# Optimization experiments

Hardware: AMD Instinct MI355X
Metric: run time of the kernel (lower is better)

## Reference

```python
import jax, jax.numpy as jnp
import numpy as np

S, NL = 64, 5000          # num_sequences, num_labels
PD, LD = 1024, 768        # protein / label embedding dims
DIM, OD = 512, 512        # latent_dim, output_dim


def setup_inputs() -> dict:
    key = jax.random.key(0)
    ks = jax.random.split(key, 8)
    sc = lambda f: 1.0 / np.sqrt(f).astype(np.float32)
    return {
        "P_f": jax.random.normal(ks[0], (S, PD), jnp.float32),
        "label_emb": jax.random.normal(ks[1], (NL, LD), jnp.float32),
        "W_p": jax.random.normal(ks[2], (DIM, PD), jnp.float32) * sc(PD),
        "W_l": jax.random.normal(ks[3], (DIM, LD), jnp.float32) * sc(LD),
        "W1": jax.random.normal(ks[4], (OD, 2 * DIM), jnp.float32) * sc(2 * DIM),
        "b1": jnp.zeros((OD,), jnp.float32),
        "W2": jax.random.normal(ks[5], (OD, OD), jnp.float32) * sc(OD),
        "b2": jnp.zeros((OD,), jnp.float32),
        "W3": jax.random.normal(ks[6], (1, OD), jnp.float32) * sc(OD),
        "b3": jnp.zeros((1,), jnp.float32),
        "L": jnp.arange(NL, dtype=jnp.int64),
    }


def reference(P_f, label_emb, W_p, W_l, W1, b1, W2, b2, W3, b3, L):
    # label lookup (cached_label_embeddings(L)) + linear projections
    L_f = label_emb[L]                      # [NL, LD]
    P_e = P_f @ W_p.T                       # [S, DIM]
    L_e = L_f @ W_l.T                       # [NL, DIM]
    # joint cat([P_e_expanded, L_e_expanded]) @ W1.T  ==  P-side + L-side GEMMs,
    # broadcast-summed (avoids materializing the [S*NL, 2*DIM] concat)
    hp = P_e @ W1[:, :DIM].T                # [S, OD]
    hl = L_e @ W1[:, DIM:].T                # [NL, OD]
    h = jax.nn.relu(hp[:, None, :] + hl[None, :, :] + b1)   # [S, NL, OD]
    h = jax.nn.relu(jnp.einsum("snd,od->sno", h, W2) + b2)  # [S, NL, OD]
    logits = jnp.einsum("sno,o->sn", h, W3[0]) + b3[0]      # [S, NL]
    return logits
```

## Files before the change

### kernel.cpp

```cpp
#include <hip/hip_runtime.h>
#include <hip/hip_bf16.h>

typedef short short8 __attribute__((ext_vector_type(8)));
typedef float f32x4 __attribute__((ext_vector_type(4)));

#define S_   64
#define NL_  5000
#define PD_  1024
#define LD_  768
#define DIM_ 512
#define OD_  512

#define BK     32
#define KSTEPS 16
#define NT_M   79
#define HL_RT  157

__device__ __forceinline__ ushort f2bf(float f) {
    union { float f; unsigned u; } v; v.f = f;
    unsigned r = v.u + 0x7fffu + ((v.u >> 16) & 1u);
    return (ushort)(r >> 16);
}
__device__ __forceinline__ float bf2f(ushort h) {
    union { unsigned u; float f; } v; v.u = ((unsigned)h) << 16;
    return v.f;
}
__device__ __forceinline__ int swz(int row, int kslot) {
    return (row * 64 + kslot * 16) ^ (((row >> 1) & 7) << 4);
}
__device__ __forceinline__ void glds16(const void* g, void* l) {
    __builtin_amdgcn_global_load_lds(
        (const __attribute__((address_space(1))) void*)g,
        (__attribute__((address_space(3))) void*)l, 16, 0, 0);
}

__device__ __forceinline__ void proj8(
    float* Af , const float* __restrict__ A, int lda, int K,
    const float* __restrict__ W, int ldw, const float* __restrict__ bias,
    float* __restrict__ C, int o0, int t) {
    const int s = t & 63, og = t >> 6;
    const int oA = o0 + og * 2, oB = oA + 1;
    float acc0 = 0.f, acc1 = 0.f;
    for (int ck = 0; ck < K; ck += 256) {
        __syncthreads();
#pragma unroll
        for (int it = 0; it < 16; it++) {
            int r = it * 4 + (t >> 6);
            float4 v = *(const float4*)(A + (size_t)r * lda + ck + (t & 63) * 4);
            *(float4*)(Af + r * 258 + (t & 63) * 4) = v;
        }
        __syncthreads();
        const float* w0 = W + (size_t)oA * ldw + ck;
        const float* w1 = W + (size_t)oB * ldw + ck;
        const float* ar = Af + s * 258;
#pragma unroll 8
        for (int k4 = 0; k4 < 64; k4++) {
            f32x4 a4 = *(const f32x4*)(ar + k4 * 4);
            float4 v0 = *(const float4*)(w0 + k4 * 4);
            float4 v1 = *(const float4*)(w1 + k4 * 4);
            acc0 += a4[0] * v0.x + a4[1] * v0.y + a4[2] * v0.z + a4[3] * v0.w;
            acc1 += a4[0] * v1.x + a4[1] * v1.y + a4[2] * v1.z + a4[3] * v1.w;
        }
    }
    C[s * DIM_ + oA] = acc0 + (bias ? bias[oA] : 0.f);
    C[s * DIM_ + oB] = acc1 + (bias ? bias[oB] : 0.f);
}

__global__ __launch_bounds__(256) void k_pre1(
    const float* __restrict__ W2, const float* __restrict__ W_l,
    const float* __restrict__ W1, const float* __restrict__ P_f,
    const float* __restrict__ W_p,
    char* __restrict__ panel, ushort* __restrict__ MlT, float* __restrict__ P_e) {
    __shared__ float lbuf[64 * 258];
    int b = blockIdx.x, t = threadIdx.x;
    if (b < 128) {
        int c = b * 256 + t;
        int o = c >> 6, rem = c & 63, kt = rem >> 2, kslot = rem & 3;
        const float* src = W2 + o * DIM_ + kt * BK + kslot * 8;
        float4 v0 = *(const float4*)src;
        float4 v1 = *(const float4*)(src + 4);
        union { ushort u[8]; short8 v; } pk;
        pk.u[0] = f2bf(v0.x); pk.u[1] = f2bf(v0.y); pk.u[2] = f2bf(v0.z); pk.u[3] = f2bf(v0.w);
        pk.u[4] = f2bf(v1.x); pk.u[5] = f2bf(v1.y); pk.u[6] = f2bf(v1.z); pk.u[7] = f2bf(v1.w);
        *(short8*)(panel + kt * 32768 + swz(o, kslot)) = pk.v;
    } else if (b < 320) {
        float (*w1r)[DIM_] = (float (*)[DIM_])lbuf;
        int bx = b - 128;
        int o0 = (bx / 3) * 8;
        int ld = (bx % 3) * 256 + t;
        for (int i = t; i < 8 * DIM_; i += 256)
            w1r[i >> 9][i & 511] = W1[(o0 + (i >> 9)) * (2 * DIM_) + DIM_ + (i & 511)];
        __syncthreads();
        float acc[8] = {};
        for (int dim = 0; dim < DIM_; dim++) {
            float wl = W_l[dim * LD_ + ld];
#pragma unroll
            for (int oi = 0; oi < 8; oi++) acc[oi] += w1r[oi][dim] * wl;
        }
#pragma unroll
        for (int oi = 0; oi < 8; oi++) MlT[(o0 + oi) * LD_ + ld] = f2bf(acc[oi]);
    } else {
        proj8(lbuf, P_f, PD_, PD_, W_p, PD_, nullptr, P_e, (b - 320) * 8, t);
    }
}

__global__ __launch_bounds__(256) void k_pre2(
    const float* __restrict__ P_e, const float* __restrict__ W1,
    const float* __restrict__ b1, const float* __restrict__ emb,
    const int* __restrict__ L, const ushort* __restrict__ MlT,
    float* __restrict__ hpb, ushort* __restrict__ hlB) {
    __shared__ float lbuf[64 * 258];
    int b = blockIdx.x, t = threadIdx.x;
    if (b < 64) {
        proj8(lbuf, P_e, DIM_, DIM_, W1, 2 * DIM_, b1, hpb, b * 8, t);
    } else {
        int hb = b - 64;
        int rblk = hb % HL_RT, oh = hb / HL_RT;
        int r0 = rblk * 32;
        int w = t >> 6, l = t & 63, lg = l >> 4, ll = l & 15;
        const float* arow[2];
#pragma unroll
        for (int mt = 0; mt < 2; mt++) {
            int r = r0 + mt * 16 + ll;
            if (r >= NL_) r = NL_ - 1;
            arow[mt] = emb + (size_t)L[r] * LD_ + lg * 8;
        }
        f32x4 acc[2][4] = {};
        for (int k = 0; k < LD_; k += 32) {
            short8 a[2], bf[4];
#pragma unroll
            for (int mt = 0; mt < 2; mt++) {
                float4 v0 = *(const float4*)(arow[mt] + k);
                float4 v1 = *(const float4*)(arow[mt] + k + 4);
                union { ushort u[8]; short8 v; } pk;
                pk.u[0] = f2bf(v0.x); pk.u[1] = f2bf(v0.y);
                pk.u[2] = f2bf(v0.z); pk.u[3] = f2bf(v0.w);
                pk.u[4] = f2bf(v1.x); pk.u[5] = f2bf(v1.y);
                pk.u[6] = f2bf(v1.z); pk.u[7] = f2bf(v1.w);
                a[mt] = pk.v;
            }
#pragma unroll
            for (int ot = 0; ot < 4; ot++) {
                int o = oh * 256 + w * 64 + ot * 16 + ll;
                bf[ot] = *(const short8*)(MlT + o * LD_ + k + lg * 8);
            }
#pragma unroll
            for (int mt = 0; mt < 2; mt++)
#pragma unroll
                for (int ot = 0; ot < 4; ot++)
                    acc[mt][ot] = __builtin_amdgcn_mfma_f32_16x16x32_bf16(a[mt], bf[ot], acc[mt][ot], 0, 0, 0);
        }
#pragma unroll
        for (int mt = 0; mt < 2; mt++)
#pragma unroll
            for (int ot = 0; ot < 4; ot++)
#pragma unroll
                for (int reg = 0; reg < 4; reg++) {
                    int r = r0 + mt * 16 + lg * 4 + reg;
                    if (r < NL_)
                        hlB[(size_t)r * DIM_ + oh * 256 + w * 64 + ot * 16 + ll] = f2bf(acc[mt][ot][reg]);
                }
    }
}

__global__ __launch_bounds__(512, 2) void k_main2(
    const ushort* __restrict__ hlB, const float* __restrict__ hpb,
    const char* __restrict__ panel, const float* __restrict__ b2,
    const float* __restrict__ W3, const float* __restrict__ b3,
    float* __restrict__ out) {
    __shared__ f32x4 ldsv[7168];
    char* lds = (char*)ldsv;
    const int t = threadIdx.x;
    const int n0 = blockIdx.x * 64, s0 = blockIdx.y * 2;
    const int w = t >> 6, lane = t & 63, lg = lane >> 4, ll = lane & 15;
    const int wr = w >> 2, wc = w & 3;

    const int arow = t >> 2, akslot = t & 3;
    int an = n0 + (arow & 63); if (an >= NL_) an = NL_ - 1;
    const ushort* hlsrc = hlB + (size_t)an * DIM_ + akslot * 8;
    const float*  hpsrc = hpb + (s0 + (arow >> 6)) * DIM_ + akslot * 8;
    const int awz = swz(arow, akslot);

    int aoffS[4], boffS[8];
#pragma unroll
    for (int mt = 0; mt < 4; mt++) aoffS[mt] = swz(wr * 64 + mt * 16 + ll, lg);
#pragma unroll
    for (int ot = 0; ot < 8; ot++) boffS[ot] = swz(wc * 128 + ot * 16 + ll, lg);

    f32x4 acc[4][8] = {};

    auto stageB = [&](int kt, int buf) {
        const char* base = panel + kt * 32768 + w * 4096 + (lane << 4);
        char* ldsB = lds + 16384 + buf * 32768 + w * 4096;
#pragma unroll
        for (int r = 0; r < 4; r++) glds16(base + r * 1024, ldsB + r * 1024);
    };
    auto packA = [&](int buf, short8 hv, float4 p0, float4 p1) {
        float hp8[8] = { p0.x, p0.y, p0.z, p0.w, p1.x, p1.y, p1.z, p1.w };
        float x[8];
#pragma unroll
        for (int e = 0; e < 8; e++) {
            float s = bf2f((ushort)hv[e]) + hp8[e];
            x[e] = s > 0.f ? s : 0.f;
        }
        union { __hip_bfloat162 h2[4]; short8 v; } pk;
#pragma unroll
        for (int e = 0; e < 4; e++)
            pk.h2[e] = __float22bfloat162_rn(make_float2(x[2 * e], x[2 * e + 1]));
        *(short8*)(lds + buf * 8192 + awz) = pk.v;
    };

    {
        short8 hv = *(const short8*)(hlsrc);
        float4 p0 = *(const float4*)(hpsrc);
        float4 p1 = *(const float4*)(hpsrc + 4);
        __builtin_amdgcn_sched_barrier(0);
        stageB(0, 0);
        stageB(1, 1);
        __builtin_amdgcn_sched_barrier(0);
        packA(0, hv, p0, p1);
        asm volatile("s_waitcnt vmcnt(4) lgkmcnt(0)" ::: "memory");
        __builtin_amdgcn_s_barrier();
    }

    for (int kt = 0; kt < KSTEPS; kt++) {
        short8 hv; float4 p0, p1;
        if (kt + 1 < KSTEPS) {
            hv = *(const short8*)(hlsrc + (kt + 1) * BK);
            p0 = *(const float4*)(hpsrc + (kt + 1) * BK);
            p1 = *(const float4*)(hpsrc + (kt + 1) * BK + 4);
        }
        __builtin_amdgcn_sched_barrier(0);
        if (kt + 2 < KSTEPS) stageB(kt + 2, (kt + 2) % 3);
        __builtin_amdgcn_sched_barrier(0);
        const char* A = lds + (kt & 1) * 8192;
        const char* B = lds + 16384 + (kt % 3) * 32768;
        short8 a[4], b[8];
#pragma unroll
        for (int mt = 0; mt < 4; mt++) a[mt] = *(const short8*)(A + aoffS[mt]);
#pragma unroll
        for (int ot = 0; ot < 8; ot++) b[ot] = *(const short8*)(B + boffS[ot]);
        __builtin_amdgcn_s_setprio(1);
#pragma unroll
        for (int mt = 0; mt < 4; mt++)
#pragma unroll
            for (int ot = 0; ot < 8; ot++)
                acc[mt][ot] = __builtin_amdgcn_mfma_f32_16x16x32_bf16(a[mt], b[ot], acc[mt][ot], 0, 0, 0);
        __builtin_amdgcn_s_setprio(0);
        if (kt + 1 < KSTEPS) packA((kt + 1) & 1, hv, p0, p1);
        asm volatile("s_waitcnt vmcnt(4) lgkmcnt(0)" ::: "memory");
        __builtin_amdgcn_s_barrier();
    }

    float* logit = (float*)lds;
    if (t < 128) logit[t] = 0.f;
    __syncthreads();
#pragma unroll
    for (int mt = 0; mt < 4; mt++) {
        float p4[4] = { 0.f, 0.f, 0.f, 0.f };
#pragma unroll
        for (int ot = 0; ot < 8; ot++) {
            int o = wc * 128 + ot * 16 + ll;
            float bb = b2[o], w3 = W3[o];
#pragma unroll
            for (int reg = 0; reg < 4; reg++) {
                float v = acc[mt][ot][reg] + bb;
                v = v > 0.f ? v : 0.f;
                p4[reg] += v * w3;
            }
        }
#pragma unroll
        for (int m = 1; m < 16; m <<= 1)
#pragma unroll
            for (int reg = 0; reg < 4; reg++) p4[reg] += __shfl_xor(p4[reg], m, 64);
        if (ll == 0)
#pragma unroll
            for (int reg = 0; reg < 4; reg++)
                atomicAdd(&logit[wr * 64 + mt * 16 + lg * 4 + reg], p4[reg]);
    }
    __syncthreads();
    if (t < 128) {
        int n = n0 + (t & 63);
        int s = s0 + (t >> 6);
        if (n < NL_) out[(size_t)s * NL_ + n] = logit[t] + b3[0];
    }
}

extern "C" void kernel_launch(void* const* d_in, const int* in_sizes, int n_in,
                              void* d_out, int out_size, void* d_ws, size_t ws_size,
                              hipStream_t stream) {
    const float* P_f = (const float*)d_in[0];
    const float* emb = (const float*)d_in[1];
    const float* W_p = (const float*)d_in[2];
    const float* W_l = (const float*)d_in[3];
    const float* W1  = (const float*)d_in[4];
    const float* b1  = (const float*)d_in[5];
    const float* W2  = (const float*)d_in[6];
    const float* b2  = (const float*)d_in[7];
    const float* W3  = (const float*)d_in[8];
    const float* b3  = (const float*)d_in[9];
    const int*   L   = (const int*)d_in[10];
    float* out = (float*)d_out;

    char* ws = (char*)d_ws;
    size_t off = 0;
    auto alloc = [&](size_t bytes) {
        void* p = ws + off;
        off = (off + bytes + 255) & ~(size_t)255;
        return p;
    };
    char*   panel = (char*)alloc((size_t)KSTEPS * 32768);
    ushort* MlT   = (ushort*)alloc((size_t)OD_ * LD_ * 2);
    float*  P_e   = (float*)alloc((size_t)S_ * DIM_ * 4);
    float*  hpb   = (float*)alloc((size_t)S_ * DIM_ * 4);
    ushort* hlB   = (ushort*)alloc((size_t)NL_ * DIM_ * 2);

    k_pre1<<<384, 256, 0, stream>>>(W2, W_l, W1, P_f, W_p, panel, MlT, P_e);
    k_pre2<<<378, 256, 0, stream>>>(P_e, W1, b1, emb, L, MlT, hpb, hlB);
    k_main2<<<dim3(NT_M, 32), 512, 0, stream>>>(hlB, hpb, panel, b2, W3, b3, out);
}
```

Baseline: 275.7 us.

## Load W2 panel fragments directly from global into registers, dropping LDS staging

The W2 bf16 panel is re-laid out so that each MFMA B-fragment is a contiguous 16-byte-per-lane chunk. The main kernel then reads B fragments straight from global memory (likely L2-resident) into registers, split into two register-buffered halves and prefetched one k-step ahead, instead of staging them through a triple-buffered LDS ring with global_load_lds. This cuts LDS use from 112KB to 16KB per block, which may allow more resident blocks, and removes the LDS B traffic. The cost is global-load latency sitting on the MFMA critical path, plus redundant per-wave global reads of the same panel.

```diff
diff --git a/kernel.cpp b/kernel.cpp
--- a/kernel.cpp
+++ b/kernel.cpp
@@ -27,11 +27,6 @@
 }
 __device__ __forceinline__ int swz(int row, int kslot) {
     return (row * 64 + kslot * 16) ^ (((row >> 1) & 7) << 4);
-}
-__device__ __forceinline__ void glds16(const void* g, void* l) {
-    __builtin_amdgcn_global_load_lds(
-        (const __attribute__((address_space(1))) void*)g,
-        (__attribute__((address_space(3))) void*)l, 16, 0, 0);
 }
 
 __device__ __forceinline__ void proj8(
@@ -82,7 +77,7 @@
         union { ushort u[8]; short8 v; } pk;
         pk.u[0] = f2bf(v0.x); pk.u[1] = f2bf(v0.y); pk.u[2] = f2bf(v0.z); pk.u[3] = f2bf(v0.w);
         pk.u[4] = f2bf(v1.x); pk.u[5] = f2bf(v1.y); pk.u[6] = f2bf(v1.z); pk.u[7] = f2bf(v1.w);
-        *(short8*)(panel + kt * 32768 + swz(o, kslot)) = pk.v;
+        *(short8*)(panel + kt * 32768 + (o >> 4) * 1024 + kslot * 256 + (o & 15) * 16) = pk.v;
     } else if (b < 320) {
         float (*w1r)[DIM_] = (float (*)[DIM_])lbuf;
         int bx = b - 128;
@@ -168,7 +163,7 @@
     const char* __restrict__ panel, const float* __restrict__ b2,
     const float* __restrict__ W3, const float* __restrict__ b3,
     float* __restrict__ out) {
-    __shared__ f32x4 ldsv[7168];
+    __shared__ f32x4 ldsv[1024];
     char* lds = (char*)ldsv;
     const int t = threadIdx.x;
     const int n0 = blockIdx.x * 64, s0 = blockIdx.y * 2;
@@ -181,20 +176,11 @@
     const float*  hpsrc = hpb + (s0 + (arow >> 6)) * DIM_ + akslot * 8;
     const int awz = swz(arow, akslot);
 
-    int aoffS[4], boffS[8];
-#pragma unroll
-    for (int mt = 0; mt < 4; mt++) aoffS[mt] = swz(wr * 64 + mt * 16 + ll, lg);
-#pragma unroll
-    for (int ot = 0; ot < 8; ot++) boffS[ot] = swz(wc * 128 + ot * 16 + ll, lg);
+    const int abase = swz(wr * 64 + ll, lg);
+    const char* bbase = panel + (wc * 8) * 1024 + lane * 16;
 
     f32x4 acc[4][8] = {};
 
-    auto stageB = [&](int kt, int buf) {
-        const char* base = panel + kt * 32768 + w * 4096 + (lane << 4);
-        char* ldsB = lds + 16384 + buf * 32768 + w * 4096;
-#pragma unroll
-        for (int r = 0; r < 4; r++) glds16(base + r * 1024, ldsB + r * 1024);
-    };
     auto packA = [&](int buf, short8 hv, float4 p0, float4 p1) {
         float hp8[8] = { p0.x, p0.y, p0.z, p0.w, p1.x, p1.y, p1.z, p1.w };
         float x[8];
@@ -214,41 +200,47 @@
         short8 hv = *(const short8*)(hlsrc);
         float4 p0 = *(const float4*)(hpsrc);
         float4 p1 = *(const float4*)(hpsrc + 4);
-        __builtin_amdgcn_sched_barrier(0);
-        stageB(0, 0);
-        stageB(1, 1);
-        __builtin_amdgcn_sched_barrier(0);
         packA(0, hv, p0, p1);
-        asm volatile("s_waitcnt vmcnt(4) lgkmcnt(0)" ::: "memory");
+        asm volatile("s_waitcnt lgkmcnt(0)" ::: "memory");
         __builtin_amdgcn_s_barrier();
     }
+    short8 bq0[4], bq1[4];
+#pragma unroll
+    for (int j = 0; j < 4; j++) bq0[j] = *(const short8*)(bbase + j * 1024);
 
     for (int kt = 0; kt < KSTEPS; kt++) {
+        const char* bkt = bbase + kt * 32768;
         short8 hv; float4 p0, p1;
         if (kt + 1 < KSTEPS) {
             hv = *(const short8*)(hlsrc + (kt + 1) * BK);
             p0 = *(const float4*)(hpsrc + (kt + 1) * BK);
             p1 = *(const float4*)(hpsrc + (kt + 1) * BK + 4);
         }
-        __builtin_amdgcn_sched_barrier(0);
-        if (kt + 2 < KSTEPS) stageB(kt + 2, (kt + 2) % 3);
-        __builtin_amdgcn_sched_barrier(0);
         const char* A = lds + (kt & 1) * 8192;
-        const char* B = lds + 16384 + (kt % 3) * 32768;
-        short8 a[4], b[8];
-#pragma unroll
-        for (int mt = 0; mt < 4; mt++) a[mt] = *(const short8*)(A + aoffS[mt]);
-#pragma unroll
-        for (int ot = 0; ot < 8; ot++) b[ot] = *(const short8*)(B + boffS[ot]);
+        short8 a[4];
+#pragma unroll
+        for (int mt = 0; mt < 4; mt++) a[mt] = *(const short8*)(A + abase + mt * 1024);
+#pragma unroll
+        for (int j = 0; j < 4; j++) bq1[j] = *(const short8*)(bkt + 4096 + j * 1024);
         __builtin_amdgcn_s_setprio(1);
 #pragma unroll
         for (int mt = 0; mt < 4; mt++)
 #pragma unroll
-            for (int ot = 0; ot < 8; ot++)
-                acc[mt][ot] = __builtin_amdgcn_mfma_f32_16x16x32_bf16(a[mt], b[ot], acc[mt][ot], 0, 0, 0);
+            for (int j = 0; j < 4; j++)
+                acc[mt][j] = __builtin_amdgcn_mfma_f32_16x16x32_bf16(a[mt], bq0[j], acc[mt][j], 0, 0, 0);
+        __builtin_amdgcn_s_setprio(0);
+        if (kt + 1 < KSTEPS)
+#pragma unroll
+            for (int j = 0; j < 4; j++) bq0[j] = *(const short8*)(bkt + 32768 + j * 1024);
+        __builtin_amdgcn_s_setprio(1);
+#pragma unroll
+        for (int mt = 0; mt < 4; mt++)
+#pragma unroll
+            for (int j = 0; j < 4; j++)
+                acc[mt][4 + j] = __builtin_amdgcn_mfma_f32_16x16x32_bf16(a[mt], bq1[j], acc[mt][4 + j], 0, 0, 0);
         __builtin_amdgcn_s_setprio(0);
         if (kt + 1 < KSTEPS) packA((kt + 1) & 1, hv, p0, p1);
-        asm volatile("s_waitcnt vmcnt(4) lgkmcnt(0)" ::: "memory");
+        asm volatile("s_waitcnt lgkmcnt(0)" ::: "memory");
         __builtin_amdgcn_s_barrier();
     }
 
```

After: 273.5 us. Within noise of the previous version (-0.8%).
